# Optimization experiments

Measured on AMD Instinct MI355X. Metric: run time of the kernel, lower is better.

## Reference

```python
import jax, jax.numpy as jnp
import numpy as np

N, F, H, C = 8192, 256, 256, 40
LP = 0.2  # LeakyReLU slope


def setup_inputs() -> dict:
    key = jax.random.key(0)
    ks = jax.random.split(key, 11)
    s = 1.0 / np.sqrt(F)
    return {
        "x": jax.random.normal(ks[0], (N, F), jnp.float32),
        "adj_f": jax.random.uniform(ks[1], (N, N), jnp.float32) / N,
        "adj_a": jax.random.uniform(ks[2], (N, N), jnp.float32) / N,
        "Wp": jax.random.normal(ks[3], (F, F), jnp.float32) * s,
        "bp": jax.random.normal(ks[4], (F,), jnp.float32) * s,
        "Wg": jax.random.normal(ks[5], (F, F), jnp.float32) * s,
        "Wb": jax.random.normal(ks[6], (F, F), jnp.float32) * s,
        "W1": jax.random.normal(ks[7], (F, H), jnp.float32) * s,
        "b1": jax.random.normal(ks[8], (H,), jnp.float32) * s,
        "W2": jax.random.normal(ks[9], (H, C), jnp.float32) * s,
        "b2": jax.random.normal(ks[10], (C,), jnp.float32) * s,
    }


def reference(x, adj_f, adj_a, Wp, bp, Wg, Wb, W1, b1, W2, b2):
    # --- DynamicPrompt.forward ---
    # GraphConvolution: adj_f @ (x @ Wp) + bp, then ReLU
    base_prompt = jax.nn.relu(adj_f @ (x @ Wp) + bp)  # [N, F]
    # adj_a.fill_diagonal_(0)
    idx = jnp.arange(N)
    adj_a0 = adj_a.at[idx, idx].set(0.0)
    neighbor = adj_a0 @ x                             # [N, F]
    gamma = jax.nn.leaky_relu(neighbor @ Wg, LP) + 1.0
    beta = jax.nn.leaky_relu(neighbor @ Wb, LP)
    learned_prompt = gamma * base_prompt + beta
    # F.normalize: L2 along dim=1, eps=1e-12
    nrm = jnp.linalg.norm(learned_prompt, axis=1, keepdims=True)
    learned_prompt = learned_prompt / jnp.maximum(nrm, 1e-12)
    # --- mix prompt into input, run frozen teacher GCN (eval: no dropout) ---
    x_in = 0.5 * (x + learned_prompt)
    h = jax.nn.relu(adj_a @ (x_in @ W1) + b1)         # gc1
    logits = adj_a @ (h @ W2) + b2                    # gc2
    return jax.nn.log_softmax(logits, axis=1)         # [N, C]
```

## Files before the change

### kernel.cpp

```cpp
#include <hip/hip_runtime.h>

typedef unsigned short u16;
typedef __attribute__((ext_vector_type(8))) short bf16x8;
typedef __attribute__((ext_vector_type(4))) float f32x4;

__device__ __forceinline__ u16 f2bf(float f) {
  union { float f; unsigned u; } v; v.f = f;
  unsigned r = v.u + 0x7FFFu + ((v.u >> 16) & 1u);
  return (u16)(r >> 16);
}
__device__ __forceinline__ float bf2f(u16 h) {
  union { unsigned u; float f; } v; v.u = ((unsigned)h) << 16; return v.f;
}
__device__ __forceinline__ unsigned pk2(float a, float b) {
  return (unsigned)f2bf(a) | ((unsigned)f2bf(b) << 16);
}
__device__ __forceinline__ unsigned cvtpk(float a, float b) {
  unsigned r;
  asm("v_cvt_pk_bf16_f32 %0, %1, %2" : "=v"(r) : "v"(a), "v"(b));
  return r;
}
__device__ __forceinline__ void gld16(const void* g, void* l) {
  __builtin_amdgcn_global_load_lds(
      (const __attribute__((address_space(1))) unsigned int*)g,
      (__attribute__((address_space(3))) unsigned int*)l, 16, 0, 0);
}

__global__ __launch_bounds__(256)
void prep_w_k(const float* __restrict__ Wp, const float* __restrict__ Wg,
              const float* __restrict__ Wb, const float* __restrict__ W1,
              const float* __restrict__ W2, u16* __restrict__ WpT,
              u16* __restrict__ WgbT, u16* __restrict__ W1T,
              u16* __restrict__ W2T) {
  int z = blockIdx.z;
  const float* in; u16* out; int C = 256;
  if (z == 0) { in = Wp; out = WpT; }
  else if (z == 1) { in = Wg; out = WgbT; }
  else if (z == 2) { in = Wb; out = WgbT + 65536; }
  else if (z == 3) { in = W1; out = W1T; }
  else { in = W2; out = W2T; C = 40; if (blockIdx.x >= 2) return; }
  __shared__ float tile[32][33];
  int tj = blockIdx.x * 32, ti = blockIdx.y * 32;
  int t = threadIdx.x, c = t & 31, r0 = t >> 5;
#pragma unroll
  for (int p = 0; p < 4; ++p) {
    int r = r0 + p * 8;
    tile[r][c] = (tj + c < C) ? in[(size_t)(ti + r) * C + (tj + c)] : 0.f;
  }
  __syncthreads();
#pragma unroll
  for (int p = 0; p < 4; ++p) {
    int rr = r0 + p * 8;
    out[(size_t)(tj + rr) * 256 + (ti + c)] = f2bf(tile[c][rr]);
  }
}

__global__ __launch_bounds__(256)
void prep_x_k(const float* __restrict__ x, const float* __restrict__ adj,
              u16* __restrict__ xT, u16* __restrict__ xbf,
              float* __restrict__ dd) {
  __shared__ float tile[32][33];
  int tj = blockIdx.x * 32, ti = blockIdx.y * 32;
  int t = threadIdx.x, c = t & 31, r0 = t >> 5;
#pragma unroll
  for (int p = 0; p < 4; ++p) {
    int r = r0 + p * 8;
    float v = x[(size_t)(ti + r) * 256 + (tj + c)];
    tile[r][c] = v;
    xbf[(size_t)(ti + r) * 256 + (tj + c)] = f2bf(v);
  }
  if (tj == 0 && t < 32) {
    int r = ti + t;
    dd[r] = bf2f(f2bf(adj[(size_t)r * 8193]));
  }
  __syncthreads();
#pragma unroll
  for (int p = 0; p < 4; ++p) {
    int rr = r0 + p * 8;
    xT[(size_t)(tj + rr) * 8192 + (ti + c)] = f2bf(tile[c][rr]);
  }
}

template <bool WRB2>
__global__ __launch_bounds__(512, 4)
void bgemm2_k(const float* __restrict__ A1, const u16* __restrict__ Bt1,
              unsigned* __restrict__ part1, const float* __restrict__ A2,
              const u16* __restrict__ Bt2, unsigned* __restrict__ part2,
              u16* __restrict__ Aout) {
  constexpr int BM = 128;
  constexpr int KP = 2048;
  constexpr int BK = 64;
  constexpr int NSTEP = KP / BK;
  constexpr int NB = 4;
  constexpr int FR = 4;
  constexpr int FC = 4;

  __shared__ u16 sA[BM * BK];
  __shared__ u16 sB[256 * BK];
  const int t = threadIdx.x, lane = t & 63, w = t >> 6;
  const int l15 = lane & 15, lhi = lane >> 4;
  const bool second = blockIdx.x >= 256;
  const float* Av = second ? A2 : A1;
  const u16* Bt = second ? Bt2 : Bt1;
  unsigned* part = second ? part2 : part1;
  const bool wrb = second && WRB2;
  const int bx = blockIdx.x & 255;
  const int xcd = bx & 7, idx = bx >> 3;
  const int kp = xcd >> 1;
  const int m = (idx << 1) | (xcd & 1);
  const int mBase = m * BM;
  const int kpBase = kp * KP;
  const int waveM = (w >> 2) * 64;
  const int waveN = (w & 3) * 64;

  f32x4 acc[FR][FC];
#pragma unroll
  for (int a = 0; a < FR; ++a)
#pragma unroll
    for (int b = 0; b < FC; ++b) acc[a][b] = (f32x4){0.f, 0.f, 0.f, 0.f};

  const int rA = t >> 2, qA = t & 3;

  for (int st = 0; st < NSTEP; ++st) {
    const int k0 = kpBase + st * BK;
#pragma unroll
    for (int i = 0; i < NB; ++i) {
      int L = i * 8192 + t * 16;
      int n = L >> 7;
      int kb = (L & 127) ^ ((n & 7) << 4);
      gld16((const char*)Bt + ((size_t)n << 14) + ((size_t)k0 << 1) + kb,
            (char*)sB + L);
    }
    {
      const float* gp = Av + ((size_t)(mBase + rA) << 13) + k0 + qA * 16;
      char* base = (char*)sA + rA * 128;
      int sw = (rA & 7) << 4;
      float4 f0 = *(const float4*)gp;
      float4 f1 = *(const float4*)(gp + 4);
      uint4 q0;
      q0.x = cvtpk(f0.x, f0.y); q0.y = cvtpk(f0.z, f0.w);
      q0.z = cvtpk(f1.x, f1.y); q0.w = cvtpk(f1.z, f1.w);
      *(uint4*)(base + ((qA * 32) ^ sw)) = q0;
      float4 f2 = *(const float4*)(gp + 8);
      float4 f3 = *(const float4*)(gp + 12);
      uint4 q1;
      q1.x = cvtpk(f2.x, f2.y); q1.y = cvtpk(f2.z, f2.w);
      q1.z = cvtpk(f3.x, f3.y); q1.w = cvtpk(f3.z, f3.w);
      *(uint4*)(base + ((qA * 32 + 16) ^ sw)) = q1;
      if (wrb) {
        u16* dst = Aout + ((size_t)(mBase + rA) << 13) + k0 + qA * 16;
        *(uint4*)dst = q0;
        *(uint4*)(dst + 8) = q1;
      }
    }
    __syncthreads();
#pragma unroll
    for (int ks = 0; ks < 2; ++ks) {
      bf16x8 av[FR], bv[FC];
#pragma unroll
      for (int fr = 0; fr < FR; ++fr) {
        int row = waveM + fr * 16 + l15;
        int off = row * 128 + ((ks * 64 + lhi * 16) ^ ((row & 7) << 4));
        av[fr] = *(const bf16x8*)((const char*)sA + off);
      }
#pragma unroll
      for (int fc = 0; fc < FC; ++fc) {
        int n = waveN + fc * 16 + l15;
        int off = n * 128 + ((ks * 64 + lhi * 16) ^ ((n & 7) << 4));
        bv[fc] = *(const bf16x8*)((const char*)sB + off);
      }
#pragma unroll
      for (int fr = 0; fr < FR; ++fr)
#pragma unroll
        for (int fc = 0; fc < FC; ++fc)
          acc[fr][fc] = __builtin_amdgcn_mfma_f32_16x16x32_bf16(
              av[fr], bv[fc], acc[fr][fc], 0, 0, 0);
    }
    __syncthreads();
  }

  unsigned* pp = part + (size_t)kp * 8192 * 128 + (size_t)mBase * 128;
#pragma unroll
  for (int fr = 0; fr < FR; ++fr)
#pragma unroll
    for (int fcp = 0; fcp < FC / 2; ++fcp) {
      int g = (waveN >> 5) + fcp;
      int r0 = waveM + fr * 16 + lhi * 4;
#pragma unroll
      for (int j = 0; j < 4; ++j)
        pp[(size_t)(r0 + j) * 128 + g * 16 + l15] =
            cvtpk(acc[fr][2 * fcp][j], acc[fr][2 * fcp + 1][j]);
    }
}

template <int BN, bool ABF, bool WRB, bool PACK>
__global__ __launch_bounds__(512, 2)
void bgemm_k(const void* __restrict__ Av, const u16* __restrict__ Bt,
             void* __restrict__ part, u16* __restrict__ Aout) {
  constexpr int BM = 64;
  constexpr int KP = 2048;
  constexpr int BK = 128;
  constexpr int NSTEP = KP / BK;
  constexpr int NB = BN / 32;
  constexpr int FR = 2;
  constexpr int FC = BN / 64;

  __shared__ u16 sA[BM * BK];
  __shared__ u16 sB[BN * BK];
  const int t = threadIdx.x, lane = t & 63, w = t >> 6;
  const int l15 = lane & 15, lhi = lane >> 4;
  const int xcd = blockIdx.x & 7, idx = blockIdx.x >> 3;
  const int kp = xcd >> 1;
  const int m = (idx << 1) | (xcd & 1);
  const int mBase = m * BM;
  const int kpBase = kp * KP;
  const int waveM = (w >> 2) * 32;
  const int waveN = (w & 3) * (BN / 4);

  f32x4 acc[FR][FC];
#pragma unroll
  for (int a = 0; a < FR; ++a)
#pragma unroll
    for (int b = 0; b < FC; ++b) acc[a][b] = (f32x4){0.f, 0.f, 0.f, 0.f};

  const int rA = t >> 3, qA = t & 7;

  for (int st = 0; st < NSTEP; ++st) {
    const int k0 = kpBase + st * BK;
#pragma unroll
    for (int i = 0; i < NB; ++i) {
      int L = i * 8192 + t * 16;
      int n = L >> 8;
      int kb = (L & 255) ^ ((n & 7) << 4);
      gld16((const char*)Bt + ((size_t)n << 14) + ((size_t)k0 << 1) + kb,
            (char*)sB + L);
    }
    if (ABF) {
#pragma unroll
      for (int i = 0; i < 2; ++i) {
        int L = i * 8192 + t * 16;
        int row = L >> 8;
        int kb = (L & 255) ^ ((row & 7) << 4);
        gld16((const char*)Av + ((size_t)(mBase + row) << 14) + ((size_t)k0 << 1) + kb,
              (char*)sA + L);
      }
    } else {
      const float* gp = (const float*)Av + ((size_t)(mBase + rA) << 13) + k0 + qA * 16;
      float4 f0 = *(const float4*)gp;
      float4 f1 = *(const float4*)(gp + 4);
      float4 f2 = *(const float4*)(gp + 8);
      float4 f3 = *(const float4*)(gp + 12);
      uint4 q0, q1;
      q0.x = cvtpk(f0.x, f0.y); q0.y = cvtpk(f0.z, f0.w);
      q0.z = cvtpk(f1.x, f1.y); q0.w = cvtpk(f1.z, f1.w);
      q1.x = cvtpk(f2.x, f2.y); q1.y = cvtpk(f2.z, f2.w);
      q1.z = cvtpk(f3.x, f3.y); q1.w = cvtpk(f3.z, f3.w);
      char* base = (char*)sA + rA * 256;
      int sw = (rA & 7) << 4;
      *(uint4*)(base + ((qA * 32) ^ sw)) = q0;
      *(uint4*)(base + ((qA * 32 + 16) ^ sw)) = q1;
      if (WRB) {
        u16* dst = Aout + ((size_t)(mBase + rA) << 13) + k0 + qA * 16;
        *(uint4*)dst = q0;
        *(uint4*)(dst + 8) = q1;
      }
    }
    __syncthreads();
#pragma unroll
    for (int ks = 0; ks < 4; ++ks) {
      bf16x8 av[FR], bv[FC];
#pragma unroll
      for (int fr = 0; fr < FR; ++fr) {
        int row = waveM + fr * 16 + l15;
        int off = row * 256 + ((ks * 64 + lhi * 16) ^ ((row & 7) << 4));
        av[fr] = *(const bf16x8*)((const char*)sA + off);
      }
#pragma unroll
      for (int fc = 0; fc < FC; ++fc) {
        int n = waveN + fc * 16 + l15;
        int off = n * 256 + ((ks * 64 + lhi * 16) ^ ((n & 7) << 4));
        bv[fc] = *(const bf16x8*)((const char*)sB + off);
      }
#pragma unroll
      for (int fr = 0; fr < FR; ++fr)
#pragma unroll
        for (int fc = 0; fc < FC; ++fc)
          acc[fr][fc] = __builtin_amdgcn_mfma_f32_16x16x32_bf16(
              av[fr], bv[fc], acc[fr][fc], 0, 0, 0);
    }
    __syncthreads();
  }

  if (PACK) {
    unsigned* pp = (unsigned*)part + (size_t)kp * 8192 * 128 + (size_t)mBase * 128;
#pragma unroll
    for (int fr = 0; fr < FR; ++fr)
#pragma unroll
      for (int fcp = 0; fcp < FC / 2; ++fcp) {
        int g = (waveN >> 5) + fcp;
        int r0 = waveM + fr * 16 + lhi * 4;
#pragma unroll
        for (int j = 0; j < 4; ++j)
          pp[(size_t)(r0 + j) * 128 + g * 16 + l15] =
              cvtpk(acc[fr][2 * fcp][j], acc[fr][2 * fcp + 1][j]);
      }
  } else {
    float* pp = (float*)part + (size_t)kp * 8192 * BN + (size_t)mBase * BN;
#pragma unroll
    for (int fr = 0; fr < FR; ++fr)
#pragma unroll
      for (int fc = 0; fc < FC; ++fc) {
        int col = waveN + fc * 16 + l15;
        int r0 = waveM + fr * 16 + lhi * 4;
#pragma unroll
        for (int j = 0; j < 4; ++j)
          pp[(size_t)(r0 + j) * BN + col] = acc[fr][fc][j];
      }
  }
}

template <int BN, int EPI, int OMODE>
__global__ __launch_bounds__(256)
void sgemm_k(const u16* __restrict__ Abf, const u16* __restrict__ Bt,
             float* __restrict__ C, int ldc, u16* __restrict__ Ct) {
  __shared__ u16 sA[32 * 256];
  __shared__ u16 sB[BN * 256];
  const int t = threadIdx.x, lane = t & 63, w = t >> 6;
  const int rowBase = blockIdx.x * 32;
  const u16* bt = Bt + (size_t)blockIdx.y * BN * 256;
  const int colBlk = blockIdx.y * BN;

#pragma unroll
  for (int i = 0; i < 4; ++i) {
    int lin = ((w * 4 + i) << 10) + (lane << 4);
    int row = lin >> 9;
    int kb = (lin & 511) ^ ((row & 7) << 4);
    const char* g = (const char*)Abf + ((size_t)(rowBase + row) << 9) + kb;
    gld16(g, (char*)sA + ((w * 4 + i) << 10));
  }
#pragma unroll
  for (int i = 0; i < BN / 8; ++i) {
    int lin = ((w * (BN / 8) + i) << 10) + (lane << 4);
    int n = lin >> 9;
    int kb = (lin & 511) ^ ((n & 7) << 4);
    const char* g = (const char*)bt + ((size_t)n << 9) + kb;
    gld16(g, (char*)sB + ((w * (BN / 8) + i) << 10));
  }
  __syncthreads();

  constexpr int FC = BN / 32;
  const int waveM = (w & 1) * 16;
  const int waveN = (w >> 1) * (BN / 2);
  f32x4 acc[FC];
#pragma unroll
  for (int b = 0; b < FC; ++b) acc[b] = (f32x4){0.f, 0.f, 0.f, 0.f};

#pragma unroll
  for (int ks = 0; ks < 8; ++ks) {
    int row = waveM + (lane & 15);
    int offA = (row * 512 + ks * 64 + ((lane >> 4) * 16)) ^ ((row & 7) << 4);
    bf16x8 av = *(const bf16x8*)((const char*)sA + offA);
#pragma unroll
    for (int fc = 0; fc < FC; ++fc) {
      int n = waveN + fc * 16 + (lane & 15);
      int offB = (n * 512 + ks * 64 + ((lane >> 4) * 16)) ^ ((n & 7) << 4);
      bf16x8 bv = *(const bf16x8*)((const char*)sB + offB);
      acc[fc] = __builtin_amdgcn_mfma_f32_16x16x32_bf16(av, bv, acc[fc], 0, 0, 0);
    }
  }

#pragma unroll
  for (int fc = 0; fc < FC; ++fc) {
    int col = waveN + fc * 16 + (lane & 15);
    int r0 = rowBase + waveM + ((lane >> 4) << 2);
    float o[4];
#pragma unroll
    for (int j = 0; j < 4; ++j) {
      float xv = acc[fc][j];
      if (EPI == 1) xv = fmaxf(xv, 0.f);
      if (EPI == 2) xv = (xv > 0.f) ? xv : 0.2f * xv;
      o[j] = xv;
    }
    if (OMODE == 1) {
      uint2 q; q.x = pk2(o[0], o[1]); q.y = pk2(o[2], o[3]);
      *(uint2*)(Ct + (size_t)(colBlk + col) * 8192 + r0) = q;
    } else if (OMODE == 2) {
#pragma unroll
      for (int j = 0; j < 4; ++j)
        Ct[(size_t)(r0 + j) * ldc + colBlk + col] = f2bf(o[j]);
    } else {
#pragma unroll
      for (int j = 0; j < 4; ++j)
        C[(size_t)(r0 + j) * ldc + colBlk + col] = o[j];
    }
  }
}

template <int MODE>
__global__ __launch_bounds__(256)
void reduce4p_k(const unsigned* __restrict__ part, const float* __restrict__ bias,
                const float* __restrict__ dd, const u16* __restrict__ xbf,
                u16* __restrict__ Cb) {
  const int tid = threadIdx.x;
  const int row = blockIdx.x * 2 + (tid >> 7);
  const int uc = tid & 127;
  const size_t S = (size_t)8192 * 128;
  const size_t b = (size_t)row * 128 + uc;
  float slo = 0.f, shi = 0.f;
#pragma unroll
  for (int p = 0; p < 4; ++p) {
    unsigned v = part[b + (size_t)p * S];
    slo += bf2f((u16)(v & 0xffff));
    shi += bf2f((u16)(v >> 16));
  }
  const int clo = (uc & 15) + ((uc >> 4) << 5), chi = clo + 16;
  if (MODE == 1) {
    float d = dd[row];
    slo -= d * bf2f(xbf[(size_t)row * 256 + clo]);
    shi -= d * bf2f(xbf[(size_t)row * 256 + chi]);
  } else {
    slo = fmaxf(slo + bias[clo], 0.f);
    shi = fmaxf(shi + bias[chi], 0.f);
  }
  Cb[(size_t)row * 256 + clo] = f2bf(slo);
  Cb[(size_t)row * 256 + chi] = f2bf(shi);
}

__global__ __launch_bounds__(128)
void fuse_red_k(const unsigned* __restrict__ part, const float* __restrict__ bp,
                const u16* __restrict__ gbuf, const u16* __restrict__ xbf,
                u16* __restrict__ xin_bf) {
  const int row = blockIdx.x, uc = threadIdx.x;
  const size_t S = (size_t)8192 * 128;
  const size_t b = (size_t)row * 128 + uc;
  float slo = 0.f, shi = 0.f;
#pragma unroll
  for (int p = 0; p < 4; ++p) {
    unsigned v = part[b + (size_t)p * S];
    slo += bf2f((u16)(v & 0xffff));
    shi += bf2f((u16)(v >> 16));
  }
  const int clo = (uc & 15) + ((uc >> 4) << 5), chi = clo + 16;
  float baselo = fmaxf(slo + bp[clo], 0.f);
  float basehi = fmaxf(shi + bp[chi], 0.f);
  float glo = bf2f(gbuf[(size_t)row * 512 + clo]);
  float ghi = bf2f(gbuf[(size_t)row * 512 + chi]);
  float btlo = bf2f(gbuf[(size_t)row * 512 + 256 + clo]);
  float bthi = bf2f(gbuf[(size_t)row * 512 + 256 + chi]);
  float lplo = (glo + 1.f) * baselo + btlo;
  float lphi = (ghi + 1.f) * basehi + bthi;
  float ss = lplo * lplo + lphi * lphi;
#pragma unroll
  for (int off = 32; off >= 1; off >>= 1) ss += __shfl_xor(ss, off);
  __shared__ float wsum[2];
  if ((uc & 63) == 0) wsum[uc >> 6] = ss;
  __syncthreads();
  float inv = 1.f / fmaxf(sqrtf(wsum[0] + wsum[1]), 1e-12f);
  xin_bf[(size_t)row * 256 + clo] =
      f2bf(0.5f * (bf2f(xbf[(size_t)row * 256 + clo]) + lplo * inv));
  xin_bf[(size_t)row * 256 + chi] =
      f2bf(0.5f * (bf2f(xbf[(size_t)row * 256 + chi]) + lphi * inv));
}

__global__ __launch_bounds__(256)
void reduce_lsm_k(const float* __restrict__ part, const float* __restrict__ b2,
                  float* __restrict__ out) {
  const int t = threadIdx.x, lane = t & 63, w = t >> 6;
  const int row = blockIdx.x * 4 + w;
  const size_t i = (size_t)row * 64 + lane;
  const size_t S = (size_t)8192 * 64;
  float v = 0.f;
#pragma unroll
  for (int p = 0; p < 4; ++p) v += part[i + (size_t)p * S];
  v = (lane < 40) ? v + b2[lane] : -1e30f;
  float mx = v;
#pragma unroll
  for (int off = 32; off >= 1; off >>= 1) mx = fmaxf(mx, __shfl_xor(mx, off));
  float e = (lane < 40) ? expf(v - mx) : 0.f;
#pragma unroll
  for (int off = 32; off >= 1; off >>= 1) e += __shfl_xor(e, off);
  float ls = mx + logf(e);
  if (lane < 40) out[(size_t)row * 40 + lane] = v - ls;
}

extern "C" void kernel_launch(void* const* d_in, const int* in_sizes, int n_in,
                              void* d_out, int out_size, void* d_ws, size_t ws_size,
                              hipStream_t stream) {
  const float* x = (const float*)d_in[0];
  const float* adj_f = (const float*)d_in[1];
  const float* adj_a = (const float*)d_in[2];
  const float* Wp = (const float*)d_in[3];
  const float* bp = (const float*)d_in[4];
  const float* Wg = (const float*)d_in[5];
  const float* Wb = (const float*)d_in[6];
  const float* W1 = (const float*)d_in[7];
  const float* b1 = (const float*)d_in[8];
  const float* W2 = (const float*)d_in[9];
  const float* b2 = (const float*)d_in[10];
  float* out = (float*)d_out;

  char* ws = (char*)d_ws;
  size_t off = 0;
  auto alloc = [&](size_t bytes) {
    char* p = ws + off;
    off += (bytes + 255) & ~(size_t)255;
    return p;
  };
  unsigned* partA = (unsigned*)alloc((size_t)4 * 8192 * 128 * 4);
  unsigned* partB = (unsigned*)alloc((size_t)4 * 8192 * 128 * 4);
  float* partBF = (float*)partB;
  u16* featT = (u16*)alloc((size_t)256 * 8192 * 2);
  u16* featT64 = (u16*)alloc((size_t)64 * 8192 * 2);
  u16* xT = (u16*)alloc((size_t)256 * 8192 * 2);
  u16* xbf = (u16*)alloc((size_t)8192 * 256 * 2);
  u16* xin_bf = (u16*)alloc((size_t)8192 * 256 * 2);
  u16* neigh_bf = (u16*)alloc((size_t)8192 * 256 * 2);
  u16* h_bf = (u16*)alloc((size_t)8192 * 256 * 2);
  u16* gbuf = (u16*)alloc((size_t)8192 * 512 * 2);
  u16* WpT = (u16*)alloc(256 * 256 * 2);
  u16* WgbT = (u16*)alloc(512 * 256 * 2);
  u16* W1T = (u16*)alloc(256 * 256 * 2);
  u16* W2T = (u16*)alloc(64 * 256 * 2);
  float* dd = (float*)alloc(8192 * 4);

  const size_t adjBytes = (size_t)8192 * 8192 * 2;
  bool useBf = (ws_size >= off + adjBytes + 256);
  u16* adj_bf = useBf ? (u16*)alloc(adjBytes) : nullptr;

  dim3 b256(256), b512(512);
  prep_w_k<<<dim3(8, 8, 5), b256, 0, stream>>>(Wp, Wg, Wb, W1, W2, WpT, WgbT, W1T, W2T);
  prep_x_k<<<dim3(8, 256), b256, 0, stream>>>(x, adj_a, xT, xbf, dd);

  sgemm_k<128, 0, 1><<<dim3(256, 2), b256, 0, stream>>>(xbf, WpT, nullptr, 0, featT);
  if (useBf)
    bgemm2_k<true><<<512, b512, 0, stream>>>(adj_f, featT, partA, adj_a, xT, partB, adj_bf);
  else
    bgemm2_k<false><<<512, b512, 0, stream>>>(adj_f, featT, partA, adj_a, xT, partB, nullptr);
  reduce4p_k<1><<<4096, b256, 0, stream>>>(partB, nullptr, dd, xbf, neigh_bf);
  sgemm_k<128, 2, 2><<<dim3(256, 4), b256, 0, stream>>>(neigh_bf, WgbT, nullptr, 512, gbuf);
  fuse_red_k<<<8192, dim3(128), 0, stream>>>(partA, bp, gbuf, xbf, xin_bf);
  sgemm_k<128, 0, 1><<<dim3(256, 2), b256, 0, stream>>>(xin_bf, W1T, nullptr, 0, featT);
  if (useBf)
    bgemm_k<256, true, false, true><<<512, b512, 0, stream>>>(adj_bf, featT, partB, nullptr);
  else
    bgemm_k<256, false, false, true><<<512, b512, 0, stream>>>(adj_a, featT, partB, nullptr);
  reduce4p_k<2><<<4096, b256, 0, stream>>>(partB, b1, nullptr, nullptr, h_bf);
  sgemm_k<64, 0, 1><<<dim3(256, 1), b256, 0, stream>>>(h_bf, W2T, nullptr, 0, featT64);
  if (useBf)
    bgemm_k<64, true, false, false><<<512, b512, 0, stream>>>(adj_bf, featT64, partB, nullptr);
  else
    bgemm_k<64, false, false, false><<<512, b512, 0, stream>>>(adj_a, featT64, partB, nullptr);
  reduce_lsm_k<<<2048, b256, 0, stream>>>(partBF, b2, out);
}
```

Measured before the change: 322.8 us.

## Double-buffer adjacency GEMMs with manual vmcnt waits and smaller row tiles

```diff
diff --git a/kernel.cpp b/kernel.cpp
--- a/kernel.cpp
+++ b/kernel.cpp
@@ -24,6 +24,13 @@
   __builtin_amdgcn_global_load_lds(
       (const __attribute__((address_space(1))) unsigned int*)g,
       (__attribute__((address_space(3))) unsigned int*)l, 16, 0, 0);
+}
+template <int N>
+__device__ __forceinline__ void waitvm() {
+  asm volatile("s_waitcnt vmcnt(%0)" ::"n"(N) : "memory");
+}
+__device__ __forceinline__ void waitlgkm0() {
+  asm volatile("s_waitcnt lgkmcnt(0)" ::: "memory");
 }
 
 __global__ __launch_bounds__(256)
@@ -81,37 +88,199 @@
   }
 }
 
+template <int BN, bool STORE, bool PACK>
+__device__ __forceinline__ void fp32_pipe(
+    const float* __restrict__ Av, const u16* __restrict__ Bt,
+    void* __restrict__ part, u16* __restrict__ Aout,
+    u16* sA, u16* sB, int mBase, int kpBase, int kp, int ph) {
+  constexpr int BK = 64;
+  constexpr int NSTEP = 2048 / BK;
+  constexpr int NB = BN / 64;
+  constexpr int S = STORE ? 1 : 0;
+  constexpr int FR = 2;
+  constexpr int FC = BN / 64;
+  const int t = threadIdx.x, lane = t & 63, w = t >> 6;
+  const int l15 = lane & 15, lhi = lane >> 4;
+  const int waveM = (w >> 2) * 32;
+  const int waveN = (w & 3) * (BN / 4);
+  const int rA = t >> 3, qA = t & 7;
+  const int swA = (rA & 7) << 4;
+
+  f32x4 acc[FR][FC];
+#pragma unroll
+  for (int a = 0; a < FR; ++a)
+#pragma unroll
+    for (int b = 0; b < FC; ++b) acc[a][b] = (f32x4){0.f, 0.f, 0.f, 0.f};
+
+  float4 a0, a1;
+  auto k0of = [&](int tt) { return kpBase + ((tt + ph) & (NSTEP - 1)) * BK; };
+  auto issueB = [&](int tt, int buf) {
+    const int k0 = k0of(tt);
+#pragma unroll
+    for (int i = 0; i < NB; ++i) {
+      int L = i * 8192 + t * 16;
+      int n = L >> 7;
+      int kb = (L & 127) ^ ((n & 7) << 4);
+      gld16((const char*)Bt + ((size_t)n << 14) + ((size_t)k0 << 1) + kb,
+            (char*)(sB + buf * (BN * 64)) + L);
+    }
+  };
+  auto issueA = [&](int tt) {
+    const float* gp = Av + ((size_t)(mBase + rA) << 13) + k0of(tt) + qA * 8;
+    a0 = *(const float4*)gp;
+    a1 = *(const float4*)(gp + 4);
+  };
+  auto writeA = [&](int tt, int buf) {
+    uint4 q;
+    q.x = cvtpk(a0.x, a0.y); q.y = cvtpk(a0.z, a0.w);
+    q.z = cvtpk(a1.x, a1.y); q.w = cvtpk(a1.z, a1.w);
+    *(uint4*)((char*)(sA + buf * 4096) + rA * 128 + ((qA * 16) ^ swA)) = q;
+    if (STORE) {
+      u16* dst = Aout + ((size_t)(mBase + rA) << 13) + k0of(tt) + qA * 8;
+      *(uint4*)dst = q;
+    }
+  };
+
+  issueA(0);
+  issueB(0, 0);
+  waitvm<NB>();
+  writeA(0, 0);
+  issueA(1);
+  waitlgkm0();
+
+  for (int tt = 0; tt < NSTEP; ++tt) {
+    const int buf = tt & 1;
+    if (tt + 1 < NSTEP) {
+      issueB(tt + 1, buf ^ 1);
+      waitvm<NB + 2 + S>();
+    } else {
+      waitvm<S>();
+    }
+    __builtin_amdgcn_s_barrier();
+    const u16* pa = sA + buf * 4096;
+    const u16* pb = sB + buf * (BN * 64);
+#pragma unroll
+    for (int ks = 0; ks < 2; ++ks) {
+      bf16x8 av[FR], bv[FC];
+#pragma unroll
+      for (int fr = 0; fr < FR; ++fr) {
+        int row = waveM + fr * 16 + l15;
+        int off = row * 128 + ((ks * 64 + lhi * 16) ^ ((row & 7) << 4));
+        av[fr] = *(const bf16x8*)((const char*)pa + off);
+      }
+#pragma unroll
+      for (int fc = 0; fc < FC; ++fc) {
+        int n = waveN + fc * 16 + l15;
+        int off = n * 128 + ((ks * 64 + lhi * 16) ^ ((n & 7) << 4));
+        bv[fc] = *(const bf16x8*)((const char*)pb + off);
+      }
+#pragma unroll
+      for (int fr = 0; fr < FR; ++fr)
+#pragma unroll
+        for (int fc = 0; fc < FC; ++fc)
+          acc[fr][fc] = __builtin_amdgcn_mfma_f32_16x16x32_bf16(
+              av[fr], bv[fc], acc[fr][fc], 0, 0, 0);
+    }
+    if (tt + 1 < NSTEP) {
+      waitvm<NB>();
+      writeA(tt + 1, buf ^ 1);
+      if (tt + 2 < NSTEP) issueA(tt + 2);
+      waitlgkm0();
+    }
+    __builtin_amdgcn_s_barrier();
+  }
+
+  if (PACK) {
+    unsigned* pp = (unsigned*)part + (size_t)kp * 8192 * 128 + (size_t)mBase * 128;
+#pragma unroll
+    for (int fr = 0; fr < FR; ++fr)
+#pragma unroll
+      for (int fcp = 0; fcp < FC / 2; ++fcp) {
+        int g = (waveN >> 5) + fcp;
+        int r0 = waveM + fr * 16 + lhi * 4;
+#pragma unroll
+        for (int j = 0; j < 4; ++j)
+          pp[(size_t)(r0 + j) * 128 + g * 16 + l15] =
+              cvtpk(acc[fr][2 * fcp][j], acc[fr][2 * fcp + 1][j]);
+      }
+  } else {
+    float* pf = (float*)part + (size_t)kp * 8192 * BN + (size_t)mBase * BN;
+#pragma unroll
+    for (int fr = 0; fr < FR; ++fr)
+#pragma unroll
+      for (int fc = 0; fc < FC; ++fc) {
+        int col = waveN + fc * 16 + l15;
+        int r0 = waveM + fr * 16 + lhi * 4;
+#pragma unroll
+        for (int j = 0; j < 4; ++j)
+          pf[(size_t)(r0 + j) * BN + col] = acc[fr][fc][j];
+      }
+  }
+}
+
 template <bool WRB2>
 __global__ __launch_bounds__(512, 4)
 void bgemm2_k(const float* __restrict__ A1, const u16* __restrict__ Bt1,
               unsigned* __restrict__ part1, const float* __restrict__ A2,
               const u16* __restrict__ Bt2, unsigned* __restrict__ part2,
               u16* __restrict__ Aout) {
-  constexpr int BM = 128;
-  constexpr int KP = 2048;
-  constexpr int BK = 64;
-  constexpr int NSTEP = KP / BK;
-  constexpr int NB = 4;
-  constexpr int FR = 4;
-  constexpr int FC = 4;
-
-  __shared__ u16 sA[BM * BK];
-  __shared__ u16 sB[256 * BK];
-  const int t = threadIdx.x, lane = t & 63, w = t >> 6;
-  const int l15 = lane & 15, lhi = lane >> 4;
-  const bool second = blockIdx.x >= 256;
-  const float* Av = second ? A2 : A1;
-  const u16* Bt = second ? Bt2 : Bt1;
-  unsigned* part = second ? part2 : part1;
-  const bool wrb = second && WRB2;
-  const int bx = blockIdx.x & 255;
+  __shared__ u16 sA[2 * 4096];
+  __shared__ u16 sB[2 * 256 * 64];
+  const bool second = blockIdx.x >= 512;
+  const int bx = blockIdx.x & 511;
+  const int ph = ((blockIdx.x >> 8) & 1) * 16;
   const int xcd = bx & 7, idx = bx >> 3;
   const int kp = xcd >> 1;
   const int m = (idx << 1) | (xcd & 1);
-  const int mBase = m * BM;
-  const int kpBase = kp * KP;
-  const int waveM = (w >> 2) * 64;
-  const int waveN = (w & 3) * 64;
+  const int mBase = m * 64;
+  const int kpBase = kp * 2048;
+  if (second) {
+    if (WRB2)
+      fp32_pipe<256, true, true>(A2, Bt2, part2, Aout, sA, sB, mBase, kpBase, kp, ph);
+    else
+      fp32_pipe<256, false, true>(A2, Bt2, part2, nullptr, sA, sB, mBase, kpBase, kp, ph);
+  } else {
+    fp32_pipe<256, false, true>(A1, Bt1, part1, nullptr, sA, sB, mBase, kpBase, kp, ph);
+  }
+}
+
+template <int BN, bool PACK>
+__global__ __launch_bounds__(512, 4)
+void bgemm_f32_k(const float* __restrict__ Av, const u16* __restrict__ Bt,
+                 void* __restrict__ part) {
+  __shared__ u16 sA[2 * 4096];
+  __shared__ u16 sB[2 * BN * 64];
+  const int bx = blockIdx.x & 511;
+  const int ph = ((blockIdx.x >> 8) & 1) * 16;
+  const int xcd = bx & 7, idx = bx >> 3;
+  const int kp = xcd >> 1;
+  const int m = (idx << 1) | (xcd & 1);
+  fp32_pipe<BN, false, PACK>(Av, Bt, part, nullptr, sA, sB, m * 64, kp * 2048, kp, ph);
+}
+
+template <int BN, bool PACK>
+__global__ __launch_bounds__(512, 4)
+void bgemm_abf_k(const u16* __restrict__ Av, const u16* __restrict__ Bt,
+                 void* __restrict__ part) {
+  constexpr int BK = 64;
+  constexpr int NSTEP = 2048 / BK;
+  constexpr int NB = BN / 64;
+  constexpr int NI = 1 + NB;
+  constexpr int FR = 2;
+  constexpr int FC = BN / 64;
+  __shared__ u16 sA[2 * 4096];
+  __shared__ u16 sB[2 * BN * 64];
+  const int t = threadIdx.x, lane = t & 63, w = t >> 6;
+  const int l15 = lane & 15, lhi = lane >> 4;
+  const int bx = blockIdx.x & 511;
+  const int ph = ((blockIdx.x >> 8) & 1) * 16;
+  const int xcd = bx & 7, idx = bx >> 3;
+  const int kp = xcd >> 1;
+  const int m = (idx << 1) | (xcd & 1);
+  const int mBase = m * 64;
+  const int kpBase = kp * 2048;
+  const int waveM = (w >> 2) * 32;
+  const int waveN = (w & 3) * (BN / 4);
 
   f32x4 acc[FR][FC];
 #pragma unroll
@@ -119,41 +288,37 @@
 #pragma unroll
     for (int b = 0; b < FC; ++b) acc[a][b] = (f32x4){0.f, 0.f, 0.f, 0.f};
 
-  const int rA = t >> 2, qA = t & 3;
-
-  for (int st = 0; st < NSTEP; ++st) {
-    const int k0 = kpBase + st * BK;
+  auto issueAB = [&](int tt, int buf) {
+    const int k0 = kpBase + ((tt + ph) & (NSTEP - 1)) * BK;
+    {
+      int L = t * 16;
+      int row = L >> 7;
+      int kb = (L & 127) ^ ((row & 7) << 4);
+      gld16((const char*)Av + ((size_t)(mBase + row) << 14) + ((size_t)k0 << 1) + kb,
+            (char*)(sA + buf * 4096) + L);
+    }
 #pragma unroll
     for (int i = 0; i < NB; ++i) {
       int L = i * 8192 + t * 16;
       int n = L >> 7;
       int kb = (L & 127) ^ ((n & 7) << 4);
       gld16((const char*)Bt + ((size_t)n << 14) + ((size_t)k0 << 1) + kb,
-            (char*)sB + L);
-    }
-    {
-      const float* gp = Av + ((size_t)(mBase + rA) << 13) + k0 + qA * 16;
-      char* base = (char*)sA + rA * 128;
-      int sw = (rA & 7) << 4;
-      float4 f0 = *(const float4*)gp;
-      float4 f1 = *(const float4*)(gp + 4);
-      uint4 q0;
-      q0.x = cvtpk(f0.x, f0.y); q0.y = cvtpk(f0.z, f0.w);
-      q0.z = cvtpk(f1.x, f1.y); q0.w = cvtpk(f1.z, f1.w);
-      *(uint4*)(base + ((qA * 32) ^ sw)) = q0;
-      float4 f2 = *(const float4*)(gp + 8);
-      float4 f3 = *(const float4*)(gp + 12);
-      uint4 q1;
-      q1.x = cvtpk(f2.x, f2.y); q1.y = cvtpk(f2.z, f2.w);
-      q1.z = cvtpk(f3.x, f3.y); q1.w = cvtpk(f3.z, f3.w);
-      *(uint4*)(base + ((qA * 32 + 16) ^ sw)) = q1;
-      if (wrb) {
-        u16* dst = Aout + ((size_t)(mBase + rA) << 13) + k0 + qA * 16;
-        *(uint4*)dst = q0;
-        *(uint4*)(dst + 8) = q1;
-      }
-    }
-    __syncthreads();
+            (char*)(sB + buf * (BN * 64)) + L);
+    }
+  };
+
+  issueAB(0, 0);
+  for (int tt = 0; tt < NSTEP; ++tt) {
+    const int buf = tt & 1;
+    if (tt + 1 < NSTEP) {
+      issueAB(tt + 1, buf ^ 1);
+      waitvm<NI>();
+    } else {
+      waitvm<0>();
+    }
+    __builtin_amdgcn_s_barrier();
+    const u16* pa = sA + buf * 4096;
+    const u16* pb = sB + buf * (BN * 64);
 #pragma unroll
     for (int ks = 0; ks < 2; ++ks) {
       bf16x8 av[FR], bv[FC];
@@ -161,13 +326,13 @@
       for (int fr = 0; fr < FR; ++fr) {
         int row = waveM + fr * 16 + l15;
         int off = row * 128 + ((ks * 64 + lhi * 16) ^ ((row & 7) << 4));
-        av[fr] = *(const bf16x8*)((const char*)sA + off);
+        av[fr] = *(const bf16x8*)((const char*)pa + off);
       }
 #pragma unroll
       for (int fc = 0; fc < FC; ++fc) {
         int n = waveN + fc * 16 + l15;
         int off = n * 128 + ((ks * 64 + lhi * 16) ^ ((n & 7) << 4));
-        bv[fc] = *(const bf16x8*)((const char*)sB + off);
+        bv[fc] = *(const bf16x8*)((const char*)pb + off);
       }
 #pragma unroll
       for (int fr = 0; fr < FR; ++fr)
@@ -176,119 +341,7 @@
           acc[fr][fc] = __builtin_amdgcn_mfma_f32_16x16x32_bf16(
               av[fr], bv[fc], acc[fr][fc], 0, 0, 0);
     }
-    __syncthreads();
-  }
-
-  unsigned* pp = part + (size_t)kp * 8192 * 128 + (size_t)mBase * 128;
-#pragma unroll
-  for (int fr = 0; fr < FR; ++fr)
-#pragma unroll
-    for (int fcp = 0; fcp < FC / 2; ++fcp) {
-      int g = (waveN >> 5) + fcp;
-      int r0 = waveM + fr * 16 + lhi * 4;
-#pragma unroll
-      for (int j = 0; j < 4; ++j)
-        pp[(size_t)(r0 + j) * 128 + g * 16 + l15] =
-            cvtpk(acc[fr][2 * fcp][j], acc[fr][2 * fcp + 1][j]);
-    }
-}
-
-template <int BN, bool ABF, bool WRB, bool PACK>
-__global__ __launch_bounds__(512, 2)
-void bgemm_k(const void* __restrict__ Av, const u16* __restrict__ Bt,
-             void* __restrict__ part, u16* __restrict__ Aout) {
-  constexpr int BM = 64;
-  constexpr int KP = 2048;
-  constexpr int BK = 128;
-  constexpr int NSTEP = KP / BK;
-  constexpr int NB = BN / 32;
-  constexpr int FR = 2;
-  constexpr int FC = BN / 64;
-
-  __shared__ u16 sA[BM * BK];
-  __shared__ u16 sB[BN * BK];
-  const int t = threadIdx.x, lane = t & 63, w = t >> 6;
-  const int l15 = lane & 15, lhi = lane >> 4;
-  const int xcd = blockIdx.x & 7, idx = blockIdx.x >> 3;
-  const int kp = xcd >> 1;
-  const int m = (idx << 1) | (xcd & 1);
-  const int mBase = m * BM;
-  const int kpBase = kp * KP;
-  const int waveM = (w >> 2) * 32;
-  const int waveN = (w & 3) * (BN / 4);
-
-  f32x4 acc[FR][FC];
-#pragma unroll
-  for (int a = 0; a < FR; ++a)
-#pragma unroll
-    for (int b = 0; b < FC; ++b) acc[a][b] = (f32x4){0.f, 0.f, 0.f, 0.f};
-
-  const int rA = t >> 3, qA = t & 7;
-
-  for (int st = 0; st < NSTEP; ++st) {
-    const int k0 = kpBase + st * BK;
-#pragma unroll
-    for (int i = 0; i < NB; ++i) {
-      int L = i * 8192 + t * 16;
-      int n = L >> 8;
-      int kb = (L & 255) ^ ((n & 7) << 4);
-      gld16((const char*)Bt + ((size_t)n << 14) + ((size_t)k0 << 1) + kb,
-            (char*)sB + L);
-    }
-    if (ABF) {
-#pragma unroll
-      for (int i = 0; i < 2; ++i) {
-        int L = i * 8192 + t * 16;
-        int row = L >> 8;
-        int kb = (L & 255) ^ ((row & 7) << 4);
-        gld16((const char*)Av + ((size_t)(mBase + row) << 14) + ((size_t)k0 << 1) + kb,
-              (char*)sA + L);
-      }
-    } else {
-      const float* gp = (const float*)Av + ((size_t)(mBase + rA) << 13) + k0 + qA * 16;
-      float4 f0 = *(const float4*)gp;
-      float4 f1 = *(const float4*)(gp + 4);
-      float4 f2 = *(const float4*)(gp + 8);
-      float4 f3 = *(const float4*)(gp + 12);
-      uint4 q0, q1;
-      q0.x = cvtpk(f0.x, f0.y); q0.y = cvtpk(f0.z, f0.w);
-      q0.z = cvtpk(f1.x, f1.y); q0.w = cvtpk(f1.z, f1.w);
-      q1.x = cvtpk(f2.x, f2.y); q1.y = cvtpk(f2.z, f2.w);
-      q1.z = cvtpk(f3.x, f3.y); q1.w = cvtpk(f3.z, f3.w);
-      char* base = (char*)sA + rA * 256;
-      int sw = (rA & 7) << 4;
-      *(uint4*)(base + ((qA * 32) ^ sw)) = q0;
-      *(uint4*)(base + ((qA * 32 + 16) ^ sw)) = q1;
-      if (WRB) {
-        u16* dst = Aout + ((size_t)(mBase + rA) << 13) + k0 + qA * 16;
-        *(uint4*)dst = q0;
-        *(uint4*)(dst + 8) = q1;
-      }
-    }
-    __syncthreads();
-#pragma unroll
-    for (int ks = 0; ks < 4; ++ks) {
-      bf16x8 av[FR], bv[FC];
-#pragma unroll
-      for (int fr = 0; fr < FR; ++fr) {
-        int row = waveM + fr * 16 + l15;
-        int off = row * 256 + ((ks * 64 + lhi * 16) ^ ((row & 7) << 4));
-        av[fr] = *(const bf16x8*)((const char*)sA + off);
-      }
-#pragma unroll
-      for (int fc = 0; fc < FC; ++fc) {
-        int n = waveN + fc * 16 + l15;
-        int off = n * 256 + ((ks * 64 + lhi * 16) ^ ((n & 7) << 4));
-        bv[fc] = *(const bf16x8*)((const char*)sB + off);
-      }
-#pragma unroll
-      for (int fr = 0; fr < FR; ++fr)
-#pragma unroll
-        for (int fc = 0; fc < FC; ++fc)
-          acc[fr][fc] = __builtin_amdgcn_mfma_f32_16x16x32_bf16(
-              av[fr], bv[fc], acc[fr][fc], 0, 0, 0);
-    }
-    __syncthreads();
+    __builtin_amdgcn_s_barrier();
   }
 
   if (PACK) {
@@ -305,7 +358,7 @@
               cvtpk(acc[fr][2 * fcp][j], acc[fr][2 * fcp + 1][j]);
       }
   } else {
-    float* pp = (float*)part + (size_t)kp * 8192 * BN + (size_t)mBase * BN;
+    float* pf = (float*)part + (size_t)kp * 8192 * BN + (size_t)mBase * BN;
 #pragma unroll
     for (int fr = 0; fr < FR; ++fr)
 #pragma unroll
@@ -314,7 +367,7 @@
         int r0 = waveM + fr * 16 + lhi * 4;
 #pragma unroll
         for (int j = 0; j < 4; ++j)
-          pp[(size_t)(r0 + j) * BN + col] = acc[fr][fc][j];
+          pf[(size_t)(r0 + j) * BN + col] = acc[fr][fc][j];
       }
   }
 }
@@ -533,22 +586,22 @@
 
   sgemm_k<128, 0, 1><<<dim3(256, 2), b256, 0, stream>>>(xbf, WpT, nullptr, 0, featT);
   if (useBf)
-    bgemm2_k<true><<<512, b512, 0, stream>>>(adj_f, featT, partA, adj_a, xT, partB, adj_bf);
+    bgemm2_k<true><<<1024, b512, 0, stream>>>(adj_f, featT, partA, adj_a, xT, partB, adj_bf);
   else
-    bgemm2_k<false><<<512, b512, 0, stream>>>(adj_f, featT, partA, adj_a, xT, partB, nullptr);
+    bgemm2_k<false><<<1024, b512, 0, stream>>>(adj_f, featT, partA, adj_a, xT, partB, nullptr);
   reduce4p_k<1><<<4096, b256, 0, stream>>>(partB, nullptr, dd, xbf, neigh_bf);
   sgemm_k<128, 2, 2><<<dim3(256, 4), b256, 0, stream>>>(neigh_bf, WgbT, nullptr, 512, gbuf);
   fuse_red_k<<<8192, dim3(128), 0, stream>>>(partA, bp, gbuf, xbf, xin_bf);
   sgemm_k<128, 0, 1><<<dim3(256, 2), b256, 0, stream>>>(xin_bf, W1T, nullptr, 0, featT);
   if (useBf)
-    bgemm_k<256, true, false, true><<<512, b512, 0, stream>>>(adj_bf, featT, partB, nullptr);
+    bgemm_abf_k<256, true><<<512, b512, 0, stream>>>(adj_bf, featT, partB);
   else
-    bgemm_k<256, false, false, true><<<512, b512, 0, stream>>>(adj_a, featT, partB, nullptr);
+    bgemm_f32_k<256, true><<<512, b512, 0, stream>>>(adj_a, featT, partB);
   reduce4p_k<2><<<4096, b256, 0, stream>>>(partB, b1, nullptr, nullptr, h_bf);
   sgemm_k<64, 0, 1><<<dim3(256, 1), b256, 0, stream>>>(h_bf, W2T, nullptr, 0, featT64);
   if (useBf)
-    bgemm_k<64, true, false, false><<<512, b512, 0, stream>>>(adj_bf, featT64, partB, nullptr);
+    bgemm_abf_k<64, false><<<512, b512, 0, stream>>>(adj_bf, featT64, partB);
   else
-    bgemm_k<64, false, false, false><<<512, b512, 0, stream>>>(adj_a, featT64, partB, nullptr);
+    bgemm_f32_k<64, false><<<512, b512, 0, stream>>>(adj_a, featT64, partB);
   reduce_lsm_k<<<2048, b256, 0, stream>>>(partBF, b2, out);
 }
```

New measurement: 312.5 us. -3.2%, faster.
